# Kernel optimization log

Hardware: AMD Instinct MI355X
Metric: run time of the kernel (lower is better)

Reference implementation:

```python
import jax, jax.numpy as jnp
import numpy as np

ITERS = 3  # iteration_num in the original module
B, L, H, N_LABELS = 16, 64, 512, 64


def setup_inputs() -> dict:
    key = jax.random.key(0)
    ks = jax.random.split(key, 11)
    s = H ** -0.5
    s2 = (2 * H) ** -0.5
    return {
        "h": jax.random.normal(ks[0], (B, L, H), jnp.float32),
        "c_slot": jax.random.normal(ks[1], (B, L, H), jnp.float32),
        "c_inte": jax.random.normal(ks[2], (B, H), jnp.float32),
        "W_SF": jax.random.normal(ks[3], (H, H), jnp.float32) * s,
        "V_SF": jax.random.normal(ks[4], (H, H), jnp.float32) * s,
        "V1_ID": jax.random.normal(ks[5], (H, H), jnp.float32) * s,
        "V2_ID_w": jax.random.normal(ks[6], (H, H), jnp.float32) * s,
        "V2_ID_b": jax.random.normal(ks[7], (H,), jnp.float32) * s,
        "W_ID": jax.random.normal(ks[8], (H, H), jnp.float32) * s,
        "W_inte_ans": jax.random.normal(ks[9], (N_LABELS, 2 * H), jnp.float32) * s2,
        "W_slot_ans": jax.random.normal(ks[10], (N_LABELS, 2 * H), jnp.float32) * s2,
    }


def reference(h, c_slot, c_inte, W_SF, V_SF, V1_ID, V2_ID_w, V2_ID_b, W_ID,
              W_inte_ans, W_slot_ans):
    # h, c_slot: [B,L,H]; c_inte: [B,H]
    # slot_features (V2_ID(h)) is loop-invariant in the original; hoisted.
    slot_features = h @ V2_ID_w.T + V2_ID_b  # [B,L,H]
    r_inte = c_inte
    r_slot = None
    for _ in range(ITERS):
        # f = sum_i V_SF(tanh(c_slot[:,i] + W_SF(r_inte))); V_SF linear -> sum first
        t = jnp.tanh(c_slot + (r_inte @ W_SF.T)[:, None, :])  # [B,L,H]
        f = t.sum(axis=1) @ V_SF.T  # [B,H]
        r_slot = f[:, None, :] * c_slot  # [B,L,H]
        hid = r_slot @ V1_ID.T  # [B,L,H]
        # pairwise additive attention scores, summed over batch AND hidden dims
        u = jnp.tanh(hid[:, :, None, :] + slot_features[:, None, :, :])  # [B,L,L,H]
        s = jnp.exp(jnp.einsum('bijh,gh->bijg', u, W_ID)).sum(axis=(0, 3))  # [L,L]
        atts = jnp.diagonal(s) / s.sum(axis=1)  # [L], scalar per position
        r = jnp.einsum('i,bih->bh', atts, r_slot)  # [B,H]
        r_inte = r + c_inte
    intent_output = jnp.concatenate([r_inte, h[:, -1, :]], axis=1) @ W_inte_ans.T  # [B,n_labels]
    slot_output = jnp.concatenate([h, r_slot], axis=-1) @ W_slot_ans.T  # [B,L,n_labels]
    return intent_output, slot_output
```

## Files before the change

kernel.cpp:

```cpp
#include <hip/hip_runtime.h>
#include <math.h>


typedef __attribute__((ext_vector_type(8))) short bf16x8;
typedef __attribute__((ext_vector_type(4))) float f32x4;

__device__ inline short f2bf(float x) {
  unsigned u = __float_as_uint(x);
  unsigned r = (u + 0x7fffu + ((u >> 16) & 1u)) >> 16;
  return (short)r;
}
__device__ inline float bf2f(short s) {
  return __uint_as_float(((unsigned)(unsigned short)s) << 16);
}
__device__ inline unsigned pack2(float a, float b) {
  return (__float_as_uint(a) >> 16) | (__float_as_uint(b) & 0xffff0000u);
}
__device__ inline float ftanh(float x) {
  float t = __expf(2.f * x);
  return 1.f - 2.f * __builtin_amdgcn_rcpf(t + 1.f);
}

__global__ __launch_bounds__(256) void k_prep(
    const float* __restrict__ W_ID, const float* __restrict__ V2,
    const float* __restrict__ V1, const float* __restrict__ W_ia,
    const float* __restrict__ W_sa, const float* __restrict__ W_SF,
    const float* __restrict__ V_SF, short* __restrict__ wbp,
    short* __restrict__ v2h, short* __restrict__ v2l,
    short* __restrict__ v1h, short* __restrict__ v1l,
    float* __restrict__ wia_t, float* __restrict__ wsa_t,
    float* __restrict__ wsf_t, float* __restrict__ vsf_t) {
  const int bx = blockIdx.x;
  const int t = threadIdx.x;
  if (bx < 1024) {
    int idx = bx * 256 + t;
    int j = idx & 7, lane = (idx >> 3) & 63;
    int ntile = (idx >> 9) & 31, kstep = idx >> 14;
    int g = ntile * 16 + (lane & 15);
    int h = kstep * 32 + (lane >> 4) * 8 + j;
    int src = g * 512 + h;
    wbp[idx] = f2bf(W_ID[src]);
    float x2 = V2[src];
    short h2 = f2bf(x2);
    v2h[idx] = h2;
    v2l[idx] = f2bf(x2 - bf2f(h2));
    float x1 = V1[src];
    short h1 = f2bf(x1);
    v1h[idx] = h1;
    v1l[idx] = f2bf(x1 - bf2f(h1));
  } else {
    const float* tin;
    float* tout;
    int R, C, c0, r0;
    if (bx < 1040) {
      tin = W_ia; tout = wia_t; R = 64; C = 1024;
      c0 = (bx - 1024) * 64; r0 = 0;
    } else if (bx < 1056) {
      tin = W_sa; tout = wsa_t; R = 64; C = 1024;
      c0 = (bx - 1040) * 64; r0 = 0;
    } else if (bx < 1120) {
      int bxx = bx - 1056;
      tin = W_SF; tout = wsf_t; R = 512; C = 512;
      c0 = (bxx & 7) * 64; r0 = (bxx >> 3) * 64;
    } else {
      int bxx = bx - 1120;
      tin = V_SF; tout = vsf_t; R = 512; C = 512;
      c0 = (bxx & 7) * 64; r0 = (bxx >> 3) * 64;
    }
    __shared__ float tile[64][65];
    const int tx = t & 63, ty = t >> 6;
#pragma unroll
    for (int it2 = 0; it2 < 16; ++it2) {
      int rl = ty + it2 * 4;
      tile[rl][tx] = tin[(r0 + rl) * C + c0 + tx];
    }
    __syncthreads();
#pragma unroll
    for (int it2 = 0; it2 < 16; ++it2) {
      int cl = ty + it2 * 4;
      tout[(c0 + cl) * R + r0 + tx] = tile[tx][cl];
    }
  }
}

__global__ __launch_bounds__(256) void k_lin(const float* __restrict__ A,
                                             const float* __restrict__ c_slot,
                                             const float* __restrict__ f,
                                             const short* __restrict__ bh,
                                             const short* __restrict__ bl,
                                             const float* __restrict__ bias,
                                             float* __restrict__ C,
                                             float* __restrict__ rs_out,
                                             float* __restrict__ smat0,
                                             float* __restrict__ fzero) {
  __shared__ short Ah[2][512], Al[2][512];
  __shared__ float fl[512];
  const int m0 = blockIdx.x * 16;
  const int nh = blockIdx.y;
  const int t = threadIdx.x;
  if (smat0 && nh == 0 && blockIdx.x < 8) {
    smat0[blockIdx.x * 512 + t] = 0.f;
    smat0[blockIdx.x * 512 + 256 + t] = 0.f;
  }
  if (fzero && nh == 1 && blockIdx.x < 16) {
    fzero[blockIdx.x * 512 + t] = 0.f;
    fzero[blockIdx.x * 512 + 256 + t] = 0.f;
  }
  if (f) {
    fl[t] = f[(blockIdx.x >> 2) * 512 + t];
    fl[t + 256] = f[(blockIdx.x >> 2) * 512 + 256 + t];
  }
  const int w = t >> 6, lane = t & 63;
  const int lq = lane >> 4, lm = lane & 15;
  f32x4 acc[2];
#pragma unroll
  for (int c = 0; c < 2; ++c) acc[c] = (f32x4){0.f, 0.f, 0.f, 0.f};

  const bf16x8* gbh = (const bf16x8*)bh + (nh * 8 + w * 2) * 64 + lane;
  const bf16x8* gbl = (const bf16x8*)bl + (nh * 8 + w * 2) * 64 + lane;

  const int la = t >> 2, j0 = (t & 3) * 2;
  const int m = la & 15, kk = (la >> 4) * 8 + j0;
  const float* abase = (f ? c_slot : A) + (m0 + m) * 512 + kk;
  float* rbase = rs_out + (m0 + m) * 512 + kk;
  if (f) __syncthreads();
  float2 x = *(const float2*)abase;

  for (int ks = 0; ks < 16; ++ks) {
    const int buf = ks & 1;
    bf16x8 b0h = gbh[ks * 2048];
    bf16x8 b1h = gbh[ks * 2048 + 64];
    bf16x8 b0l = gbl[ks * 2048];
    bf16x8 b1l = gbl[ks * 2048 + 64];
    float2 xn = x;
    if (ks < 15) xn = *(const float2*)(abase + (ks + 1) * 32);
    float a0 = x.x, a1 = x.y;
    if (f) {
      a0 *= fl[ks * 32 + kk];
      a1 *= fl[ks * 32 + kk + 1];
      if (nh == 0) *(float2*)(rbase + ks * 32) = make_float2(a0, a1);
    }
    short h0 = f2bf(a0), h1 = f2bf(a1);
    short l0 = f2bf(a0 - bf2f(h0)), l1 = f2bf(a1 - bf2f(h1));
    *(short2*)&Ah[buf][t * 2] = make_short2(h0, h1);
    *(short2*)&Al[buf][t * 2] = make_short2(l0, l1);
    __syncthreads();
    bf16x8 ah = *(const bf16x8*)&Ah[buf][lane * 8];
    bf16x8 al = *(const bf16x8*)&Al[buf][lane * 8];
    acc[0] = __builtin_amdgcn_mfma_f32_16x16x32_bf16(ah, b0h, acc[0], 0, 0, 0);
    acc[0] = __builtin_amdgcn_mfma_f32_16x16x32_bf16(al, b0h, acc[0], 0, 0, 0);
    acc[0] = __builtin_amdgcn_mfma_f32_16x16x32_bf16(ah, b0l, acc[0], 0, 0, 0);
    acc[1] = __builtin_amdgcn_mfma_f32_16x16x32_bf16(ah, b1h, acc[1], 0, 0, 0);
    acc[1] = __builtin_amdgcn_mfma_f32_16x16x32_bf16(al, b1h, acc[1], 0, 0, 0);
    acc[1] = __builtin_amdgcn_mfma_f32_16x16x32_bf16(ah, b1l, acc[1], 0, 0, 0);
    x = xn;
  }
#pragma unroll
  for (int c = 0; c < 2; ++c)
#pragma unroll
    for (int reg = 0; reg < 4; ++reg) {
      int mm = m0 + lq * 4 + reg;
      int n = nh * 128 + (w * 2 + c) * 16 + lm;
      float v = acc[c][reg];
      if (bias) v += bias[n];
      C[mm * 512 + n] = v;
    }
}

__global__ __launch_bounds__(512) void k_mid(int first,
                                             const float* __restrict__ smat,
                                             const float* __restrict__ r_slot,
                                             const float* __restrict__ c_inte,
                                             const float* __restrict__ c_slot,
                                             const float* __restrict__ wsf_t,
                                             const float* __restrict__ vsf_t,
                                             float* __restrict__ f) {
  __shared__ float av[64];
  __shared__ float riv[512];
  __shared__ float red[512];
  __shared__ float tm[64], ts[64];
  const int b = blockIdx.x >> 3, hc = blockIdx.x & 7;
  const int t = threadIdx.x;
  const int hl = t & 63, kq = t >> 6;

  if (first) {
    riv[t] = c_inte[b * 512 + t];
  } else {
    if (t < 256) {
      int w = t >> 6, lane = t & 63;
      for (int r = w * 16; r < w * 16 + 16; ++r) {
        float v = smat[r * 64 + lane];
        float s = v;
        s += __shfl_xor(s, 1);
        s += __shfl_xor(s, 2);
        s += __shfl_xor(s, 4);
        s += __shfl_xor(s, 8);
        s += __shfl_xor(s, 16);
        s += __shfl_xor(s, 32);
        float d = __shfl(v, r);
        if (lane == 0) av[r] = d / s;
      }
    }
    __syncthreads();
    float a = 0.f;
    const float* rp = r_slot + b * 64 * 512 + t;
#pragma unroll 8
    for (int i = 0; i < 64; ++i) a += av[i] * rp[i * 512];
    riv[t] = a + c_inte[b * 512 + t];
  }
  __syncthreads();
  {
    const float* wp = wsf_t + hc * 64 + hl;
    float p = 0.f;
#pragma unroll 8
    for (int k = kq * 64; k < kq * 64 + 64; ++k) p += riv[k] * wp[k * 512];
    red[t] = p;
  }
  __syncthreads();
  if (t < 64) {
    float s = 0.f;
#pragma unroll
    for (int q = 0; q < 8; ++q) s += red[q * 64 + t];
    tm[t] = s;
  }
  __syncthreads();
  {
    float tmph = tm[hl];
    const float* cp = c_slot + (b * 64 + kq * 8) * 512 + hc * 64 + hl;
    float s = 0.f;
#pragma unroll
    for (int l = 0; l < 8; ++l) s += ftanh(cp[l * 512] + tmph);
    red[t] = s;
  }
  __syncthreads();
  if (t < 64) {
    float s = 0.f;
#pragma unroll
    for (int q = 0; q < 8; ++q) s += red[q * 64 + t];
    ts[t] = s;
  }
  __syncthreads();
  {
    const float* vp = vsf_t + (hc * 64) * 512 + t;
    float p = 0.f;
#pragma unroll 8
    for (int k = 0; k < 64; ++k) p += ts[k] * vp[k * 512];
    atomicAdd(&f[b * 512 + t], p);
  }
}

__global__ __launch_bounds__(512, 4) void k_score(const float* __restrict__ hid,
                                                  const float* __restrict__ sf,
                                                  const short* __restrict__ wbp,
                                                  float* __restrict__ smat,
                                                  float* __restrict__ fz,
                                                  float* __restrict__ oz) {
  __shared__ short As[16][2048];
  __shared__ float red[8][64];
  const int i = blockIdx.x, b = blockIdx.y;
  const int t = threadIdx.x;
  if (fz && i == 0) fz[b * 512 + t] = 0.f;
  if (oz && i == 1 && b < 2) oz[b * 512 + t] = 0.f;
  const int w = t >> 6, lane = t & 63;
  const int lq = lane >> 4, lm = lane & 15;

  f32x4 acc[4][4];
#pragma unroll
  for (int r = 0; r < 4; ++r)
#pragma unroll
    for (int c = 0; c < 4; ++c) acc[r][c] = (f32x4){0.f, 0.f, 0.f, 0.f};

  const float* hrow = hid + (b * 64 + i) * 512;
  const float* sfb = sf + b * 64 * 512;

  const int fid = t >> 1, half = t & 1;
  const int am = (fid >> 6) * 16 + (fid & 15);
  const int ak = ((fid >> 4) & 3) * 8 + half * 4;
  const int aoff = fid * 8 + half * 4;

  const float* hp0 = hrow + ak;
  const float* sp0 = sfb + am * 512 + ak;

#pragma unroll 4
  for (int ks = 0; ks < 16; ++ks) {
    float4 hv = *(const float4*)(hp0 + ks * 32);
    float4 sv = *(const float4*)(sp0 + ks * 32);
    uint2 pk;
    pk.x = pack2(ftanh(hv.x + sv.x), ftanh(hv.y + sv.y));
    pk.y = pack2(ftanh(hv.z + sv.z), ftanh(hv.w + sv.w));
    *(uint2*)&As[ks][aoff] = pk;
  }
  __syncthreads();

  const bf16x8* gb = (const bf16x8*)wbp + (w * 4) * 64 + lane;
  bf16x8 nb0 = gb[0];
  bf16x8 nb1 = gb[64];
  bf16x8 nb2 = gb[128];
  bf16x8 nb3 = gb[192];
  for (int ks = 0; ks < 16; ++ks) {
    bf16x8 b0 = nb0, b1 = nb1, b2 = nb2, b3 = nb3;
    if (ks < 15) {
      nb0 = gb[(ks + 1) * 2048];
      nb1 = gb[(ks + 1) * 2048 + 64];
      nb2 = gb[(ks + 1) * 2048 + 128];
      nb3 = gb[(ks + 1) * 2048 + 192];
    }
    bf16x8 af0 = *(const bf16x8*)&As[ks][(0 * 64 + lane) * 8];
    bf16x8 af1 = *(const bf16x8*)&As[ks][(1 * 64 + lane) * 8];
    bf16x8 af2 = *(const bf16x8*)&As[ks][(2 * 64 + lane) * 8];
    bf16x8 af3 = *(const bf16x8*)&As[ks][(3 * 64 + lane) * 8];
    acc[0][0] = __builtin_amdgcn_mfma_f32_16x16x32_bf16(af0, b0, acc[0][0], 0, 0, 0);
    acc[1][0] = __builtin_amdgcn_mfma_f32_16x16x32_bf16(af1, b0, acc[1][0], 0, 0, 0);
    acc[2][0] = __builtin_amdgcn_mfma_f32_16x16x32_bf16(af2, b0, acc[2][0], 0, 0, 0);
    acc[3][0] = __builtin_amdgcn_mfma_f32_16x16x32_bf16(af3, b0, acc[3][0], 0, 0, 0);
    acc[0][1] = __builtin_amdgcn_mfma_f32_16x16x32_bf16(af0, b1, acc[0][1], 0, 0, 0);
    acc[1][1] = __builtin_amdgcn_mfma_f32_16x16x32_bf16(af1, b1, acc[1][1], 0, 0, 0);
    acc[2][1] = __builtin_amdgcn_mfma_f32_16x16x32_bf16(af2, b1, acc[2][1], 0, 0, 0);
    acc[3][1] = __builtin_amdgcn_mfma_f32_16x16x32_bf16(af3, b1, acc[3][1], 0, 0, 0);
    acc[0][2] = __builtin_amdgcn_mfma_f32_16x16x32_bf16(af0, b2, acc[0][2], 0, 0, 0);
    acc[1][2] = __builtin_amdgcn_mfma_f32_16x16x32_bf16(af1, b2, acc[1][2], 0, 0, 0);
    acc[2][2] = __builtin_amdgcn_mfma_f32_16x16x32_bf16(af2, b2, acc[2][2], 0, 0, 0);
    acc[3][2] = __builtin_amdgcn_mfma_f32_16x16x32_bf16(af3, b2, acc[3][2], 0, 0, 0);
    acc[0][3] = __builtin_amdgcn_mfma_f32_16x16x32_bf16(af0, b3, acc[0][3], 0, 0, 0);
    acc[1][3] = __builtin_amdgcn_mfma_f32_16x16x32_bf16(af1, b3, acc[1][3], 0, 0, 0);
    acc[2][3] = __builtin_amdgcn_mfma_f32_16x16x32_bf16(af2, b3, acc[2][3], 0, 0, 0);
    acc[3][3] = __builtin_amdgcn_mfma_f32_16x16x32_bf16(af3, b3, acc[3][3], 0, 0, 0);
  }

#pragma unroll
  for (int r = 0; r < 4; ++r) {
#pragma unroll
    for (int reg = 0; reg < 4; ++reg) {
      float v = __expf(acc[r][0][reg]) + __expf(acc[r][1][reg]) +
                __expf(acc[r][2][reg]) + __expf(acc[r][3][reg]);
      v += __shfl_down(v, 8, 16);
      v += __shfl_down(v, 4, 16);
      v += __shfl_down(v, 2, 16);
      v += __shfl_down(v, 1, 16);
      if (lm == 0) red[w][r * 16 + lq * 4 + reg] = v;
    }
  }
  __syncthreads();
  if (t < 64) {
    float s = 0.f;
#pragma unroll
    for (int ww = 0; ww < 8; ++ww) s += red[ww][t];
    atomicAdd(&smat[i * 64 + t], s);
  }
}

__global__ __launch_bounds__(256) void k_post(const float* __restrict__ smat,
                                              const float* __restrict__ r_slot,
                                              const float* __restrict__ c_inte,
                                              const float* __restrict__ h,
                                              const float* __restrict__ wia_t,
                                              const float* __restrict__ wsa_t,
                                              float* __restrict__ out) {
  __shared__ float av[64], riv[64], red[256];
  const int t = threadIdx.x;
  if (blockIdx.x < 256) {
    int idx = blockIdx.x * 256 + t;
    int ml = idx >> 6, n = idx & 63;
    const float* x1 = h + ml * 512;
    const float* x2 = r_slot + ml * 512;
    float acc = 0.f;
    for (int k = 0; k < 512; k += 4) {
      float4 x = *(const float4*)(x1 + k);
      acc += x.x * wsa_t[k * 64 + n] + x.y * wsa_t[(k + 1) * 64 + n] +
             x.z * wsa_t[(k + 2) * 64 + n] + x.w * wsa_t[(k + 3) * 64 + n];
    }
    for (int k = 0; k < 512; k += 4) {
      float4 x = *(const float4*)(x2 + k);
      acc += x.x * wsa_t[(512 + k) * 64 + n] + x.y * wsa_t[(513 + k) * 64 + n] +
             x.z * wsa_t[(514 + k) * 64 + n] + x.w * wsa_t[(515 + k) * 64 + n];
    }
    out[1024 + idx] = acc;
  } else {
    const int bb = blockIdx.x - 256;
    const int b = bb >> 3, kc = bb & 7;
    const int w = t >> 6, lane = t & 63;
    for (int r = w * 16; r < w * 16 + 16; ++r) {
      float v = smat[r * 64 + lane];
      float s = v;
      s += __shfl_xor(s, 1);
      s += __shfl_xor(s, 2);
      s += __shfl_xor(s, 4);
      s += __shfl_xor(s, 8);
      s += __shfl_xor(s, 16);
      s += __shfl_xor(s, 32);
      float d = __shfl(v, r);
      if (lane == 0) av[r] = d / s;
    }
    __syncthreads();
    {
      const int hh = kc * 64 + lane;
      float a = 0.f;
      const float* rp = r_slot + (b * 64 + w * 16) * 512 + hh;
#pragma unroll
      for (int i = 0; i < 16; ++i) a += av[w * 16 + i] * rp[i * 512];
      red[t] = a;
    }
    __syncthreads();
    if (t < 64)
      riv[t] = red[t] + red[t + 64] + red[t + 128] + red[t + 192] +
               c_inte[b * 512 + kc * 64 + t];
    __syncthreads();
    {
      const int n = lane;
      const float* hrow = h + (b * 64 + 63) * 512 + kc * 64;
      float p = 0.f;
#pragma unroll
      for (int k = w * 16; k < w * 16 + 16; ++k) {
        p += riv[k] * wia_t[(kc * 64 + k) * 64 + n];
        p += hrow[k] * wia_t[(512 + kc * 64 + k) * 64 + n];
      }
      red[t] = p;
    }
    __syncthreads();
    if (t < 64)
      atomicAdd(&out[b * 64 + t],
                red[t] + red[t + 64] + red[t + 128] + red[t + 192]);
  }
}

extern "C" void kernel_launch(void* const* d_in, const int* in_sizes, int n_in,
                              void* d_out, int out_size, void* d_ws, size_t ws_size,
                              hipStream_t stream) {
  const float* h      = (const float*)d_in[0];
  const float* c_slot = (const float*)d_in[1];
  const float* c_inte = (const float*)d_in[2];
  const float* W_SF   = (const float*)d_in[3];
  const float* V_SF   = (const float*)d_in[4];
  const float* V1_ID  = (const float*)d_in[5];
  const float* V2_w   = (const float*)d_in[6];
  const float* V2_b   = (const float*)d_in[7];
  const float* W_ID   = (const float*)d_in[8];
  const float* W_ia   = (const float*)d_in[9];
  const float* W_sa   = (const float*)d_in[10];
  float* out = (float*)d_out;

  float* ws     = (float*)d_ws;
  short* wbp    = (short*)ws;
  short* v2h    = (short*)(ws + 131072);
  short* v2l    = (short*)(ws + 262144);
  short* v1h    = (short*)(ws + 393216);
  short* v1l    = (short*)(ws + 524288);
  float* sfbuf  = ws + 655360;
  float* r_slot = ws + 1179648;
  float* hid    = ws + 1703936;
  float* smat   = ws + 2228224;
  float* f      = ws + 2232320;
  float* wia_t  = ws + 2240512;
  float* wsa_t  = ws + 2306048;
  float* wsf_t  = ws + 2371584;
  float* vsf_t  = ws + 2633728;

  k_prep<<<1184, 256, 0, stream>>>(W_ID, V2_w, V1_ID, W_ia, W_sa, W_SF, V_SF,
                                   wbp, v2h, v2l, v1h, v1l,
                                   wia_t, wsa_t, wsf_t, vsf_t);
  k_lin<<<dim3(64, 4), 256, 0, stream>>>(h, nullptr, nullptr, v2h, v2l, V2_b,
                                         sfbuf, r_slot, nullptr, f);

  for (int it = 0; it < 3; ++it) {
    k_mid<<<128, 512, 0, stream>>>(it == 0 ? 1 : 0, smat, r_slot, c_inte,
                                   c_slot, wsf_t, vsf_t, f);
    k_lin<<<dim3(64, 4), 256, 0, stream>>>(nullptr, c_slot, f, v1h, v1l,
                                           nullptr, hid, r_slot, smat, nullptr);
    k_score<<<dim3(64, 16), 512, 0, stream>>>(hid, sfbuf, wbp, smat, f,
                                              it == 2 ? out : nullptr);
  }

  k_post<<<384, 256, 0, stream>>>(smat, r_slot, c_inte, h, wia_t, wsa_t, out);
}
```

Before: 306.3 us.

## Fuse weight prep into first linear kernel and split V2 on the fly

Merges the separate weight-preparation kernel into the first slot-feature GEMM launch, with extra grid rows doing the W_ID/V1 packing and the transposes while the GEMM blocks run. The V2 weight is no longer pre-split into bf16 hi/lo buffers; the GEMM reads raw fp32 rows and splits them in registers, removing a launch and a round trip through workspace. The iteration GEMM is specialized into its own kernel without null-pointer branches, and the W_ID fragment prefetch in the score kernel is moved before the tanh staging loop. The cost is more global fp32 traffic and per-element conversion work inside the first GEMM.

New measurement: 301.5 us, median of 2. Within noise of the previous version (-1.6%).

```diff
diff --git a/kernel.cpp b/kernel.cpp
--- a/kernel.cpp
+++ b/kernel.cpp
@@ -20,130 +20,130 @@
   float t = __expf(2.f * x);
   return 1.f - 2.f * __builtin_amdgcn_rcpf(t + 1.f);
 }
-
-__global__ __launch_bounds__(256) void k_prep(
-    const float* __restrict__ W_ID, const float* __restrict__ V2,
-    const float* __restrict__ V1, const float* __restrict__ W_ia,
-    const float* __restrict__ W_sa, const float* __restrict__ W_SF,
-    const float* __restrict__ V_SF, short* __restrict__ wbp,
-    short* __restrict__ v2h, short* __restrict__ v2l,
-    short* __restrict__ v1h, short* __restrict__ v1l,
+__device__ inline void split8(float4 a, float4 b, bf16x8* hi, bf16x8* lo) {
+  float xs[8] = {a.x, a.y, a.z, a.w, b.x, b.y, b.z, b.w};
+  bf16x8 h, l;
+#pragma unroll
+  for (int e = 0; e < 8; ++e) {
+    short hh = f2bf(xs[e]);
+    h[e] = hh;
+    l[e] = f2bf(xs[e] - bf2f(hh));
+  }
+  *hi = h;
+  *lo = l;
+}
+
+__global__ __launch_bounds__(256) void k_lin1(
+    const float* __restrict__ A, const float* __restrict__ rawB,
+    const float* __restrict__ bias, float* __restrict__ C,
+    const float* __restrict__ W_ID, const float* __restrict__ V1,
+    const float* __restrict__ W_ia, const float* __restrict__ W_sa,
+    const float* __restrict__ W_SF, const float* __restrict__ V_SF,
+    short* __restrict__ wbp, short* __restrict__ v1h, short* __restrict__ v1l,
     float* __restrict__ wia_t, float* __restrict__ wsa_t,
-    float* __restrict__ wsf_t, float* __restrict__ vsf_t) {
-  const int bx = blockIdx.x;
-  const int t = threadIdx.x;
-  if (bx < 1024) {
-    int idx = bx * 256 + t;
-    int j = idx & 7, lane = (idx >> 3) & 63;
-    int ntile = (idx >> 9) & 31, kstep = idx >> 14;
-    int g = ntile * 16 + (lane & 15);
-    int h = kstep * 32 + (lane >> 4) * 8 + j;
-    int src = g * 512 + h;
-    wbp[idx] = f2bf(W_ID[src]);
-    float x2 = V2[src];
-    short h2 = f2bf(x2);
-    v2h[idx] = h2;
-    v2l[idx] = f2bf(x2 - bf2f(h2));
-    float x1 = V1[src];
-    short h1 = f2bf(x1);
-    v1h[idx] = h1;
-    v1l[idx] = f2bf(x1 - bf2f(h1));
-  } else {
-    const float* tin;
-    float* tout;
-    int R, C, c0, r0;
-    if (bx < 1040) {
-      tin = W_ia; tout = wia_t; R = 64; C = 1024;
-      c0 = (bx - 1024) * 64; r0 = 0;
-    } else if (bx < 1056) {
-      tin = W_sa; tout = wsa_t; R = 64; C = 1024;
-      c0 = (bx - 1040) * 64; r0 = 0;
-    } else if (bx < 1120) {
-      int bxx = bx - 1056;
-      tin = W_SF; tout = wsf_t; R = 512; C = 512;
-      c0 = (bxx & 7) * 64; r0 = (bxx >> 3) * 64;
-    } else {
-      int bxx = bx - 1120;
-      tin = V_SF; tout = vsf_t; R = 512; C = 512;
-      c0 = (bxx & 7) * 64; r0 = (bxx >> 3) * 64;
-    }
-    __shared__ float tile[64][65];
-    const int tx = t & 63, ty = t >> 6;
-#pragma unroll
-    for (int it2 = 0; it2 < 16; ++it2) {
-      int rl = ty + it2 * 4;
-      tile[rl][tx] = tin[(r0 + rl) * C + c0 + tx];
-    }
-    __syncthreads();
-#pragma unroll
-    for (int it2 = 0; it2 < 16; ++it2) {
-      int cl = ty + it2 * 4;
-      tout[(c0 + cl) * R + r0 + tx] = tile[tx][cl];
-    }
-  }
-}
-
-__global__ __launch_bounds__(256) void k_lin(const float* __restrict__ A,
-                                             const float* __restrict__ c_slot,
-                                             const float* __restrict__ f,
-                                             const short* __restrict__ bh,
-                                             const short* __restrict__ bl,
-                                             const float* __restrict__ bias,
-                                             float* __restrict__ C,
-                                             float* __restrict__ rs_out,
-                                             float* __restrict__ smat0,
-                                             float* __restrict__ fzero) {
+    float* __restrict__ wsf_t, float* __restrict__ vsf_t,
+    float* __restrict__ fzero) {
   __shared__ short Ah[2][512], Al[2][512];
-  __shared__ float fl[512];
-  const int m0 = blockIdx.x * 16;
+  __shared__ float tile[64][65];
   const int nh = blockIdx.y;
   const int t = threadIdx.x;
-  if (smat0 && nh == 0 && blockIdx.x < 8) {
-    smat0[blockIdx.x * 512 + t] = 0.f;
-    smat0[blockIdx.x * 512 + 256 + t] = 0.f;
-  }
+
+  if (nh >= 4) {
+    const int pid = (nh - 4) * 64 + blockIdx.x;
+    if (pid < 256) {
+#pragma unroll
+      for (int e = 0; e < 4; ++e) {
+        int idx = pid * 1024 + e * 256 + t;
+        int j = idx & 7, lane = (idx >> 3) & 63;
+        int ntile = (idx >> 9) & 31, kstep = idx >> 14;
+        int g = ntile * 16 + (lane & 15);
+        int h = kstep * 32 + (lane >> 4) * 8 + j;
+        wbp[idx] = f2bf(W_ID[g * 512 + h]);
+      }
+    } else if (pid < 512) {
+      int p = pid - 256;
+#pragma unroll
+      for (int e = 0; e < 4; ++e) {
+        int idx = p * 1024 + e * 256 + t;
+        int j = idx & 7, lane = (idx >> 3) & 63;
+        int ntile = (idx >> 9) & 31, kstep = idx >> 14;
+        int g = ntile * 16 + (lane & 15);
+        int h = kstep * 32 + (lane >> 4) * 8 + j;
+        float x = V1[g * 512 + h];
+        short hi = f2bf(x);
+        v1h[idx] = hi;
+        v1l[idx] = f2bf(x - bf2f(hi));
+      }
+    } else if (pid < 672) {
+      int p = pid - 512;
+      const float* tin;
+      float* tout;
+      int R, C2, c0, r0;
+      if (p < 64) {
+        tin = W_SF; tout = wsf_t; R = 512; C2 = 512;
+        c0 = (p & 7) * 64; r0 = (p >> 3) * 64;
+      } else if (p < 128) {
+        int q = p - 64;
+        tin = V_SF; tout = vsf_t; R = 512; C2 = 512;
+        c0 = (q & 7) * 64; r0 = (q >> 3) * 64;
+      } else if (p < 144) {
+        tin = W_ia; tout = wia_t; R = 64; C2 = 1024;
+        c0 = (p - 128) * 64; r0 = 0;
+      } else {
+        tin = W_sa; tout = wsa_t; R = 64; C2 = 1024;
+        c0 = (p - 144) * 64; r0 = 0;
+      }
+      const int tx = t & 63, ty = t >> 6;
+#pragma unroll
+      for (int it2 = 0; it2 < 16; ++it2) {
+        int rl = ty + it2 * 4;
+        tile[rl][tx] = tin[(r0 + rl) * C2 + c0 + tx];
+      }
+      __syncthreads();
+#pragma unroll
+      for (int it2 = 0; it2 < 16; ++it2) {
+        int cl = ty + it2 * 4;
+        tout[(c0 + cl) * R + r0 + tx] = tile[tx][cl];
+      }
+    }
+    return;
+  }
+
+  const int m0 = blockIdx.x * 16;
   if (fzero && nh == 1 && blockIdx.x < 16) {
     fzero[blockIdx.x * 512 + t] = 0.f;
     fzero[blockIdx.x * 512 + 256 + t] = 0.f;
   }
-  if (f) {
-    fl[t] = f[(blockIdx.x >> 2) * 512 + t];
-    fl[t + 256] = f[(blockIdx.x >> 2) * 512 + 256 + t];
-  }
   const int w = t >> 6, lane = t & 63;
   const int lq = lane >> 4, lm = lane & 15;
   f32x4 acc[2];
 #pragma unroll
   for (int c = 0; c < 2; ++c) acc[c] = (f32x4){0.f, 0.f, 0.f, 0.f};
 
-  const bf16x8* gbh = (const bf16x8*)bh + (nh * 8 + w * 2) * 64 + lane;
-  const bf16x8* gbl = (const bf16x8*)bl + (nh * 8 + w * 2) * 64 + lane;
+  const int nt0 = nh * 8 + w * 2;
+  const float* vb0 = rawB + (nt0 * 16 + lm) * 512 + lq * 8;
+  const float* vb1 = vb0 + 16 * 512;
 
   const int la = t >> 2, j0 = (t & 3) * 2;
   const int m = la & 15, kk = (la >> 4) * 8 + j0;
-  const float* abase = (f ? c_slot : A) + (m0 + m) * 512 + kk;
-  float* rbase = rs_out + (m0 + m) * 512 + kk;
-  if (f) __syncthreads();
+  const float* abase = A + (m0 + m) * 512 + kk;
   float2 x = *(const float2*)abase;
 
   for (int ks = 0; ks < 16; ++ks) {
     const int buf = ks & 1;
-    bf16x8 b0h = gbh[ks * 2048];
-    bf16x8 b1h = gbh[ks * 2048 + 64];
-    bf16x8 b0l = gbl[ks * 2048];
-    bf16x8 b1l = gbl[ks * 2048 + 64];
+    float4 q0 = *(const float4*)(vb0 + ks * 32);
+    float4 q1 = *(const float4*)(vb0 + ks * 32 + 4);
+    float4 p0 = *(const float4*)(vb1 + ks * 32);
+    float4 p1 = *(const float4*)(vb1 + ks * 32 + 4);
     float2 xn = x;
     if (ks < 15) xn = *(const float2*)(abase + (ks + 1) * 32);
-    float a0 = x.x, a1 = x.y;
-    if (f) {
-      a0 *= fl[ks * 32 + kk];
-      a1 *= fl[ks * 32 + kk + 1];
-      if (nh == 0) *(float2*)(rbase + ks * 32) = make_float2(a0, a1);
-    }
-    short h0 = f2bf(a0), h1 = f2bf(a1);
-    short l0 = f2bf(a0 - bf2f(h0)), l1 = f2bf(a1 - bf2f(h1));
+    short h0 = f2bf(x.x), h1 = f2bf(x.y);
+    short l0 = f2bf(x.x - bf2f(h0)), l1 = f2bf(x.y - bf2f(h1));
     *(short2*)&Ah[buf][t * 2] = make_short2(h0, h1);
     *(short2*)&Al[buf][t * 2] = make_short2(l0, l1);
+    bf16x8 b0h, b0l, b1h, b1l;
+    split8(q0, q1, &b0h, &b0l);
+    split8(p0, p1, &b1h, &b1l);
     __syncthreads();
     bf16x8 ah = *(const bf16x8*)&Ah[buf][lane * 8];
     bf16x8 al = *(const bf16x8*)&Al[buf][lane * 8];
@@ -160,10 +160,78 @@
 #pragma unroll
     for (int reg = 0; reg < 4; ++reg) {
       int mm = m0 + lq * 4 + reg;
+      int n = (nt0 + c) * 16 + lm;
+      C[mm * 512 + n] = acc[c][reg] + bias[n];
+    }
+}
+
+__global__ __launch_bounds__(256) void k_lin(const float* __restrict__ c_slot,
+                                             const float* __restrict__ f,
+                                             const short* __restrict__ bh,
+                                             const short* __restrict__ bl,
+                                             float* __restrict__ C,
+                                             float* __restrict__ rs_out,
+                                             float* __restrict__ smat0) {
+  __shared__ short Ah[2][512], Al[2][512];
+  __shared__ float fl[512];
+  const int m0 = blockIdx.x * 16;
+  const int nh = blockIdx.y;
+  const int t = threadIdx.x;
+  if (nh == 0 && blockIdx.x < 8) {
+    smat0[blockIdx.x * 512 + t] = 0.f;
+    smat0[blockIdx.x * 512 + 256 + t] = 0.f;
+  }
+  fl[t] = f[(blockIdx.x >> 2) * 512 + t];
+  fl[t + 256] = f[(blockIdx.x >> 2) * 512 + 256 + t];
+  const int w = t >> 6, lane = t & 63;
+  const int lq = lane >> 4, lm = lane & 15;
+  f32x4 acc[2];
+#pragma unroll
+  for (int c = 0; c < 2; ++c) acc[c] = (f32x4){0.f, 0.f, 0.f, 0.f};
+
+  const bf16x8* gbh = (const bf16x8*)bh + (nh * 8 + w * 2) * 64 + lane;
+  const bf16x8* gbl = (const bf16x8*)bl + (nh * 8 + w * 2) * 64 + lane;
+
+  const int la = t >> 2, j0 = (t & 3) * 2;
+  const int m = la & 15, kk = (la >> 4) * 8 + j0;
+  const float* abase = c_slot + (m0 + m) * 512 + kk;
+  float* rbase = rs_out + (m0 + m) * 512 + kk;
+  __syncthreads();
+  float2 x = *(const float2*)abase;
+
+  for (int ks = 0; ks < 16; ++ks) {
+    const int buf = ks & 1;
+    bf16x8 b0h = gbh[ks * 2048];
+    bf16x8 b1h = gbh[ks * 2048 + 64];
+    bf16x8 b0l = gbl[ks * 2048];
+    bf16x8 b1l = gbl[ks * 2048 + 64];
+    float2 xn = x;
+    if (ks < 15) xn = *(const float2*)(abase + (ks + 1) * 32);
+    float a0 = x.x * fl[ks * 32 + kk];
+    float a1 = x.y * fl[ks * 32 + kk + 1];
+    if (nh == 0) *(float2*)(rbase + ks * 32) = make_float2(a0, a1);
+    short h0 = f2bf(a0), h1 = f2bf(a1);
+    short l0 = f2bf(a0 - bf2f(h0)), l1 = f2bf(a1 - bf2f(h1));
+    *(short2*)&Ah[buf][t * 2] = make_short2(h0, h1);
+    *(short2*)&Al[buf][t * 2] = make_short2(l0, l1);
+    __syncthreads();
+    bf16x8 ah = *(const bf16x8*)&Ah[buf][lane * 8];
+    bf16x8 al = *(const bf16x8*)&Al[buf][lane * 8];
+    acc[0] = __builtin_amdgcn_mfma_f32_16x16x32_bf16(ah, b0h, acc[0], 0, 0, 0);
+    acc[0] = __builtin_amdgcn_mfma_f32_16x16x32_bf16(al, b0h, acc[0], 0, 0, 0);
+    acc[0] = __builtin_amdgcn_mfma_f32_16x16x32_bf16(ah, b0l, acc[0], 0, 0, 0);
+    acc[1] = __builtin_amdgcn_mfma_f32_16x16x32_bf16(ah, b1h, acc[1], 0, 0, 0);
+    acc[1] = __builtin_amdgcn_mfma_f32_16x16x32_bf16(al, b1h, acc[1], 0, 0, 0);
+    acc[1] = __builtin_amdgcn_mfma_f32_16x16x32_bf16(ah, b1l, acc[1], 0, 0, 0);
+    x = xn;
+  }
+#pragma unroll
+  for (int c = 0; c < 2; ++c)
+#pragma unroll
+    for (int reg = 0; reg < 4; ++reg) {
+      int mm = m0 + lq * 4 + reg;
       int n = nh * 128 + (w * 2 + c) * 16 + lm;
-      float v = acc[c][reg];
-      if (bias) v += bias[n];
-      C[mm * 512 + n] = v;
+      C[mm * 512 + n] = acc[c][reg];
     }
 }
 
@@ -281,6 +349,12 @@
   const float* hp0 = hrow + ak;
   const float* sp0 = sfb + am * 512 + ak;
 
+  const bf16x8* gb = (const bf16x8*)wbp + (w * 4) * 64 + lane;
+  bf16x8 nb0 = gb[0];
+  bf16x8 nb1 = gb[64];
+  bf16x8 nb2 = gb[128];
+  bf16x8 nb3 = gb[192];
+
 #pragma unroll 4
   for (int ks = 0; ks < 16; ++ks) {
     float4 hv = *(const float4*)(hp0 + ks * 32);
@@ -292,11 +366,6 @@
   }
   __syncthreads();
 
-  const bf16x8* gb = (const bf16x8*)wbp + (w * 4) * 64 + lane;
-  bf16x8 nb0 = gb[0];
-  bf16x8 nb1 = gb[64];
-  bf16x8 nb2 = gb[128];
-  bf16x8 nb3 = gb[192];
   for (int ks = 0; ks < 16; ++ks) {
     bf16x8 b0 = nb0, b1 = nb1, b2 = nb2, b3 = nb3;
     if (ks < 15) {
@@ -441,8 +510,6 @@
 
   float* ws     = (float*)d_ws;
   short* wbp    = (short*)ws;
-  short* v2h    = (short*)(ws + 131072);
-  short* v2l    = (short*)(ws + 262144);
   short* v1h    = (short*)(ws + 393216);
   short* v1l    = (short*)(ws + 524288);
   float* sfbuf  = ws + 655360;
@@ -455,17 +522,16 @@
   float* wsf_t  = ws + 2371584;
   float* vsf_t  = ws + 2633728;
 
-  k_prep<<<1184, 256, 0, stream>>>(W_ID, V2_w, V1_ID, W_ia, W_sa, W_SF, V_SF,
-                                   wbp, v2h, v2l, v1h, v1l,
-                                   wia_t, wsa_t, wsf_t, vsf_t);
-  k_lin<<<dim3(64, 4), 256, 0, stream>>>(h, nullptr, nullptr, v2h, v2l, V2_b,
-                                         sfbuf, r_slot, nullptr, f);
+  k_lin1<<<dim3(64, 15), 256, 0, stream>>>(h, V2_w, V2_b, sfbuf,
+                                           W_ID, V1_ID, W_ia, W_sa, W_SF, V_SF,
+                                           wbp, v1h, v1l,
+                                           wia_t, wsa_t, wsf_t, vsf_t, f);
 
   for (int it = 0; it < 3; ++it) {
     k_mid<<<128, 512, 0, stream>>>(it == 0 ? 1 : 0, smat, r_slot, c_inte,
                                    c_slot, wsf_t, vsf_t, f);
-    k_lin<<<dim3(64, 4), 256, 0, stream>>>(nullptr, c_slot, f, v1h, v1l,
-                                           nullptr, hid, r_slot, smat, nullptr);
+    k_lin<<<dim3(64, 4), 256, 0, stream>>>(c_slot, f, v1h, v1l,
+                                           hid, r_slot, smat);
     k_score<<<dim3(64, 16), 512, 0, stream>>>(hid, sfbuf, wbp, smat, f,
                                               it == 2 ? out : nullptr);
   }
```
